# Kernel optimization log

Hardware: AMD Instinct MI355X
Metric: run time of the kernel (lower is better)

The kernel has to match this reference:

```python
import jax, jax.numpy as jnp
import numpy as np

HEADS = 8
SR = 2
EPS_BN = 1e-5
EPS_LN = 1e-5


def _conv(x, w, b, stride=1, pad=0):
    y = jax.lax.conv_general_dilated(x, w, (stride, stride), [(pad, pad), (pad, pad)],
                                     dimension_numbers=('NCHW', 'OIHW', 'NCHW'))
    return y + b[None, :, None, None]


def _bn(x, g, b):
    # eval-mode BatchNorm with running_mean=0, running_var=1
    return x * (g / jnp.sqrt(1.0 + EPS_BN))[None, :, None, None] + b[None, :, None, None]


def _dwt_haar(x):
    # [B,c,H,W] -> [B,4c,H/2,W/2] stacked as LL,HL,LH,HH (Wave-ViT convention)
    x1 = x[:, :, 0::2, 0::2] / 2
    x2 = x[:, :, 1::2, 0::2] / 2
    x3 = x[:, :, 0::2, 1::2] / 2
    x4 = x[:, :, 1::2, 1::2] / 2
    ll = x1 + x2 + x3 + x4
    hl = -x1 - x2 + x3 + x4
    lh = -x1 + x2 - x3 + x4
    hh = x1 - x2 - x3 + x4
    return jnp.concatenate([ll, hl, lh, hh], axis=1)


def _idwt_haar(y):
    # [B,4c,h,w] -> [B,c,2h,2w], exact inverse of _dwt_haar
    c = y.shape[1] // 4
    ll, hl, lh, hh = y[:, :c], y[:, c:2 * c], y[:, 2 * c:3 * c], y[:, 3 * c:]
    p1 = (ll - hl - lh + hh) / 2  # (0::2, 0::2)
    p2 = (ll - hl + lh - hh) / 2  # (1::2, 0::2)
    p3 = (ll + hl - lh - hh) / 2  # (0::2, 1::2)
    p4 = (ll + hl + lh + hh) / 2  # (1::2, 1::2)
    B, _, h2, w2 = ll.shape
    row0 = jnp.stack([p1, p3], axis=-1)  # even rows
    row1 = jnp.stack([p2, p4], axis=-1)  # odd rows
    out = jnp.stack([row0, row1], axis=3)  # [B,c,h2,2,w2,2]
    return out.reshape(B, c, 2 * h2, 2 * w2)


def setup_inputs() -> dict:
    key = jax.random.key(0)
    ks = jax.random.split(key, 12)
    B, H, W, C = 8, 56, 56, 512
    N = H * W
    c4 = C // 4

    def nrm(k, shp, std):
        return jax.random.normal(k, shp, jnp.float32) * std

    return {
        'x': jax.random.normal(ks[0], (B, N, C), jnp.float32),
        'H': H, 'W': W,
        'reduce_w': nrm(ks[1], (c4, C, 1, 1), (2.0 / c4) ** 0.5),
        'reduce_b': jnp.zeros((c4,), jnp.float32),
        'reduce_g': jnp.ones((c4,), jnp.float32),
        'reduce_beta': jnp.zeros((c4,), jnp.float32),
        'filter_w': nrm(ks[2], (C, C, 3, 3), (2.0 / (9 * C)) ** 0.5),
        'filter_b': jnp.zeros((C,), jnp.float32),
        'filter_g': jnp.ones((C,), jnp.float32),
        'filter_beta': jnp.zeros((C,), jnp.float32),
        'q_w': nrm(ks[3], (C, C), 0.02),
        'q_b': jnp.zeros((C,), jnp.float32),
        'ln_g': jnp.ones((C,), jnp.float32),
        'ln_b': jnp.zeros((C,), jnp.float32),
        'kv_w': nrm(ks[4], (2 * C, C), 0.02),
        'kv_b': jnp.zeros((2 * C,), jnp.float32),
        'kve_w': nrm(ks[5], (C, C, SR, SR), (2.0 / (SR * SR * C)) ** 0.5),
        'kve_b': jnp.zeros((C,), jnp.float32),
        'proj_w': nrm(ks[6], (C, C + c4), 0.02),
        'proj_b': jnp.zeros((C,), jnp.float32),
    }


def reference(x, H, W, reduce_w, reduce_b, reduce_g, reduce_beta,
              filter_w, filter_b, filter_g, filter_beta,
              q_w, q_b, ln_g, ln_b, kv_w, kv_b, kve_w, kve_b, proj_w, proj_b):
    B, N, C = x.shape
    hd = C // HEADS
    scale = hd ** -0.5

    q = (x @ q_w.T + q_b).reshape(B, N, HEADS, hd).transpose(0, 2, 1, 3)  # [B,h,N,d]

    xi = x.reshape(B, H, W, C).transpose(0, 3, 1, 2)  # NCHW
    r = jax.nn.relu(_bn(_conv(xi, reduce_w, reduce_b), reduce_g, reduce_beta))  # [B,C/4,H,W]
    r16 = r.astype(jnp.float16)
    x_dwt = _dwt_haar(r16).astype(jnp.float32)  # [B,C,H/2,W/2]
    x_dwt = jax.nn.relu(_bn(_conv(x_dwt, filter_w, filter_b, pad=1), filter_g, filter_beta))
    x_dwt16 = x_dwt.astype(jnp.float16)
    x_idwt = _idwt_haar(x_dwt16)  # [B,C/4,H,W] fp16
    x_idwt = x_idwt.reshape(B, C // 4, H * W).transpose(0, 2, 1)  # [B,N,C/4]

    x_dwt = x_dwt16.astype(jnp.float32)
    kv_in = _conv(x_dwt, kve_w, kve_b, stride=SR).reshape(B, C, -1).transpose(0, 2, 1)  # [B,M,C]
    mu = kv_in.mean(-1, keepdims=True)
    var = ((kv_in - mu) ** 2).mean(-1, keepdims=True)
    kv_n = (kv_in - mu) / jnp.sqrt(var + EPS_LN) * ln_g + ln_b
    kv = (kv_n @ kv_w.T + kv_b).reshape(B, -1, 2, HEADS, hd).transpose(2, 0, 3, 1, 4)
    k, v = kv[0], kv[1]  # [B,h,M,d]

    attn = jax.nn.softmax(jnp.einsum('bhnd,bhmd->bhnm', q, k) * scale, axis=-1)
    o = jnp.einsum('bhnm,bhmd->bhnd', attn, v).transpose(0, 2, 1, 3).reshape(B, N, C)
    o = jnp.concatenate([o, x_idwt.astype(jnp.float32)], axis=-1)  # [B,N,C+C/4]
    return o @ proj_w.T + proj_b
```

## Files before the change

### kernel.cpp

```cpp
#include <hip/hip_runtime.h>
#include <math.h>


typedef _Float16 half8 __attribute__((ext_vector_type(8)));
typedef _Float16 half4v __attribute__((ext_vector_type(4)));
typedef float f32x4 __attribute__((ext_vector_type(4)));

static const size_t OFF_X16  = 0;
static const size_t OFF_Q16  = 12845056;
static const size_t OFF_CAT  = 25690112;
static const size_t OFF_R16  = 41746432;
static const size_t OFF_PAD  = 44957696;
static const size_t OFF_DWTB = 48644096;
static const size_t OFF_QRW  = 51855360;
static const size_t OFF_LN16 = 55066624;
static const size_t OFF_KV16 = 55869440;
static const size_t OFF_WT   = 57475072;
static const size_t OFF_KT   = 59834368;
static const size_t OFF_QW   = 60882944;
static const size_t OFF_KVW  = 61145088;
static const size_t OFF_PW   = 61669376;
static const size_t OFF_RW   = 61997056;
static const size_t OFF_VT   = 62062592;
static const size_t OFF_PART = 62980096;

#define BN_RSQ 0.9999950000374997f
#define SCL2   0.1803368801111204f
#define PART_STRIDE 3211264
#define KVE_STRIDE  802816

__device__ __forceinline__ void async_copy16(const _Float16* g, _Float16* l) {
    __builtin_amdgcn_global_load_lds(
        (const __attribute__((address_space(1))) void*)g,
        (__attribute__((address_space(3))) void*)l, 16, 0, 0);
}

#define WAIT4_BARRIER() asm volatile("s_waitcnt vmcnt(4)\n\ts_barrier" ::: "memory")
#define WAIT0_BARRIER() asm volatile("s_waitcnt vmcnt(0)\n\ts_barrier" ::: "memory")

template <int ALOAD, int EPI>
__global__ __launch_bounds__(256) void gemm16(
    const _Float16* __restrict__ A, const _Float16* __restrict__ W,
    void* __restrict__ outp, int M, int K, int lda, int ldc,
    const float* __restrict__ bias, const float* __restrict__ bng,
    const float* __restrict__ bnb, const float* __restrict__ bias2,
    void* __restrict__ outp2)
{
    __shared__ _Float16 sA[3][128 * 32];
    __shared__ _Float16 sB[3][128 * 32];
    const int t = threadIdx.x;
    const int lane = t & 63, wid = t >> 6;

    int bx = blockIdx.x, by = blockIdx.y;
    {
        int nwg = gridDim.x * gridDim.y;
        if ((nwg & 7) == 0) {
            int orig = by * gridDim.x + bx;
            int cs = nwg >> 3;
            int wg = (orig & 7) * cs + (orig >> 3);
            by = wg % gridDim.y;
            bx = wg / gridDim.y;
        }
    }
    const int m0 = bx * 128, n0 = by * 128;
    const int kbase = blockIdx.z * K;

    const int sr = wid * 16 + (lane >> 2);
    const int sc = (lane & 3) * 8;
    const int stA0 = wid * 512;
    const int stA1 = 2048 + wid * 512;

    const _Float16 *aP0, *aP1;
    if constexpr (ALOAD == 0) {
        int r0 = m0 + sr;      if (r0 > M - 1) r0 = M - 1;
        int r1 = m0 + 64 + sr; if (r1 > M - 1) r1 = M - 1;
        aP0 = A + (size_t)r0 * lda + sc;
        aP1 = A + (size_t)r1 * lda + sc;
    } else {
        int m_ = m0 + sr; if (m_ > M - 1) m_ = M - 1;
        int b_ = m_ / 196, rem = m_ - b_ * 196, i_ = rem / 14, j_ = rem - i_ * 14;
        aP0 = A + ((size_t)(b_ * 784 + 2 * i_ * 28 + 2 * j_)) * 512 + sc;
        m_ = m0 + 64 + sr; if (m_ > M - 1) m_ = M - 1;
        b_ = m_ / 196; rem = m_ - b_ * 196; i_ = rem / 14; j_ = rem - i_ * 14;
        aP1 = A + ((size_t)(b_ * 784 + 2 * i_ * 28 + 2 * j_)) * 512 + sc;
    }
    const int ldw = (ALOAD == 2) ? lda : K;
    const _Float16* bP0 = W + (size_t)(n0 + sr) * ldw + sc;
    const _Float16* bP1 = W + (size_t)(n0 + 64 + sr) * ldw + sc;

    const int mw = wid & 1, nw = wid >> 1;
    const int pAoff = (mw * 64 + (lane & 15)) * 32 + (lane >> 4) * 8;
    const int pBoff = (nw * 64 + (lane & 15)) * 32 + (lane >> 4) * 8;

    f32x4 acc[4][4];
#pragma unroll
    for (int i = 0; i < 4; ++i)
#pragma unroll
        for (int j = 0; j < 4; ++j) acc[i][j] = (f32x4)(0.0f);

    auto aoff_of = [&](int k) -> int {
        if constexpr (ALOAD == 0) {
            return k;
        } else {
            int sub = k >> 9; int ky = sub >> 1, kx = sub & 1;
            return (ky * 28 + kx) * 512 + (k & 511);
        }
    };
    auto stage = [&](int ti, int buf) {
        int k = kbase + ti * 32;
        int aOff = aoff_of(k);
        async_copy16(aP0 + aOff, &sA[buf][stA0]);
        async_copy16(aP1 + aOff, &sA[buf][stA1]);
        async_copy16(bP0 + k, &sB[buf][stA0]);
        async_copy16(bP1 + k, &sB[buf][stA1]);
    };

    const int nt = K >> 5;
    stage(0, 0);
    if (nt > 1) { stage(1, 1); WAIT4_BARRIER(); }
    else        { WAIT0_BARRIER(); }

    int cur = 0;
    for (int i = 0; i < nt; ++i) {
        const _Float16* pA = &sA[cur][0] + pAoff;
        const _Float16* pB = &sB[cur][0] + pBoff;
        half8 aF[4], bF[4];
#pragma unroll
        for (int u = 0; u < 4; ++u) aF[u] = *(const half8*)(pA + u * 512);
#pragma unroll
        for (int u = 0; u < 4; ++u) bF[u] = *(const half8*)(pB + u * 512);

        const bool st = (i + 2 < nt);
        if (st) {
            int nb = cur + 2; if (nb >= 3) nb -= 3;
            stage(i + 2, nb);
        }
#pragma unroll
        for (int u = 0; u < 4; ++u)
#pragma unroll
            for (int j = 0; j < 4; ++j)
                acc[u][j] = __builtin_amdgcn_mfma_f32_16x16x32_f16(
                    aF[u], bF[j], acc[u][j], 0, 0, 0);

        if (i + 1 < nt) {
            if (st) WAIT4_BARRIER();
            else    WAIT0_BARRIER();
        }
        ++cur; if (cur == 3) cur = 0;
    }

    const int orow = m0 + mw * 64 + (lane >> 4) * 4;
    const int ocol = n0 + nw * 64 + (lane & 15);
#pragma unroll
    for (int j = 0; j < 4; ++j) {
        int col = ocol + j * 16;
        float bv = 0.0f, g = 0.0f, b2 = 0.0f;
        if constexpr (EPI == 4) {
            if (n0 >= 512) {
                bv = bias2[col - 512];
                g = bng[col - 512] * BN_RSQ;
                b2 = bnb[col - 512];
            } else {
                bv = bias[col];
            }
        } else if constexpr (EPI != 3) {
            bv = bias[col];
        }
        if constexpr (EPI == 1) { g = bng[col] * BN_RSQ; b2 = bnb[col]; }
#pragma unroll
        for (int i = 0; i < 4; ++i) {
#pragma unroll
            for (int r = 0; r < 4; ++r) {
                int row = orow + i * 16 + r;
                if (row >= M) continue;
                float v = acc[i][j][r] + bv;
                if constexpr (EPI == 1) v = fmaxf(v * g + b2, 0.0f);
                if constexpr (EPI == 0) {
                    __builtin_nontemporal_store(
                        v, (float*)outp + (size_t)row * ldc + col);
                } else if constexpr (EPI == 3) {
                    __builtin_nontemporal_store(
                        v, (float*)outp + (size_t)blockIdx.z * KVE_STRIDE
                           + (size_t)row * ldc + col);
                } else if constexpr (EPI == 4) {
                    if (n0 >= 512) {
                        v = fmaxf(v * g + b2, 0.0f);
                        ((_Float16*)outp2)[(size_t)row * 128 + (col - 512)] =
                            (_Float16)v;
                    } else {
                        ((_Float16*)outp)[(size_t)row * ldc + col] = (_Float16)v;
                    }
                } else {
                    ((_Float16*)outp)[(size_t)row * ldc + col] = (_Float16)v;
                }
            }
        }
    }
}

__global__ __launch_bounds__(256) void conv_splitk(
    const _Float16* __restrict__ A, const _Float16* __restrict__ W,
    float* __restrict__ partA, float* __restrict__ partB)
{
    __shared__ _Float16 sA[3][128 * 32];
    __shared__ _Float16 sB[3][128 * 32];
    const int t = threadIdx.x;
    const int lane = t & 63, wid = t >> 6;

    int orig = blockIdx.x;
    int wg = (orig & 7) * 98 + (orig >> 3);
    int bx = wg % 49;  int c = wg / 49;
    int by = c & 3,    bz = c >> 2;

    const int m0 = bx * 128, n0 = by * 128;
    const int kbase = bz * 1152;

    const int sr = wid * 16 + (lane >> 2);
    const int sc = (lane & 3) * 8;
    const int stA0 = wid * 512;
    const int stA1 = 2048 + wid * 512;

    int m_ = m0 + sr;
    int b_ = m_ / 784, rem = m_ - b_ * 784, y_ = rem / 28, x_ = rem - y_ * 28;
    const _Float16* aP0 = A + ((size_t)(b_ * 900 + (y_ + 1) * 30 + (x_ + 1))) * 512 + sc;
    m_ = m0 + 64 + sr;
    b_ = m_ / 784; rem = m_ - b_ * 784; y_ = rem / 28; x_ = rem - y_ * 28;
    const _Float16* aP1 = A + ((size_t)(b_ * 900 + (y_ + 1) * 30 + (x_ + 1))) * 512 + sc;
    const _Float16* bP0 = W + (size_t)(n0 + sr) * 4608 + sc;
    const _Float16* bP1 = W + (size_t)(n0 + 64 + sr) * 4608 + sc;

    const int mw = wid & 1, nw = wid >> 1;
    const int pAoff = (mw * 64 + (lane & 15)) * 32 + (lane >> 4) * 8;
    const int pBoff = (nw * 64 + (lane & 15)) * 32 + (lane >> 4) * 8;

    f32x4 acc[4][4];
#pragma unroll
    for (int i = 0; i < 4; ++i)
#pragma unroll
        for (int j = 0; j < 4; ++j) acc[i][j] = (f32x4)(0.0f);

    auto aoff_of = [&](int k) -> int {
        int sub = k >> 9; int s3 = sub / 3;
        int dy = s3 - 1, dx = sub - s3 * 3 - 1;
        return (dy * 30 + dx) * 512 + (k & 511);
    };
    auto stage = [&](int ti, int buf) {
        int k = kbase + ti * 32;
        int aOff = aoff_of(k);
        async_copy16(aP0 + aOff, &sA[buf][stA0]);
        async_copy16(aP1 + aOff, &sA[buf][stA1]);
        async_copy16(bP0 + k, &sB[buf][stA0]);
        async_copy16(bP1 + k, &sB[buf][stA1]);
    };

    const int nt = 36;
    stage(0, 0);
    stage(1, 1);
    WAIT4_BARRIER();

    int cur = 0;
    for (int i = 0; i < nt; ++i) {
        const _Float16* pA = &sA[cur][0] + pAoff;
        const _Float16* pB = &sB[cur][0] + pBoff;
        half8 aF[4], bF[4];
#pragma unroll
        for (int u = 0; u < 4; ++u) aF[u] = *(const half8*)(pA + u * 512);
#pragma unroll
        for (int u = 0; u < 4; ++u) bF[u] = *(const half8*)(pB + u * 512);

        const bool st = (i + 2 < nt);
        if (st) {
            int nb = cur + 2; if (nb >= 3) nb -= 3;
            stage(i + 2, nb);
        }
#pragma unroll
        for (int u = 0; u < 4; ++u)
#pragma unroll
            for (int j = 0; j < 4; ++j)
                acc[u][j] = __builtin_amdgcn_mfma_f32_16x16x32_f16(
                    aF[u], bF[j], acc[u][j], 0, 0, 0);

        if (i + 1 < nt) {
            if (st) WAIT4_BARRIER();
            else    WAIT0_BARRIER();
        }
        ++cur; if (cur == 3) cur = 0;
    }

    float* dst = (bz < 2) ? (partA + (size_t)bz * PART_STRIDE)
                          : (partB + (size_t)(bz - 2) * PART_STRIDE);
    const int orow = m0 + mw * 64 + (lane >> 4) * 4;
    const int ocol = n0 + nw * 64 + (lane & 15);
#pragma unroll
    for (int j = 0; j < 4; ++j) {
#pragma unroll
        for (int i = 0; i < 4; ++i)
#pragma unroll
            for (int r = 0; r < 4; ++r)
                __builtin_nontemporal_store(
                    acc[i][j][r],
                    &dst[(size_t)(orow + i * 16 + r) * 512 + ocol + j * 16]);
    }
}

__global__ __launch_bounds__(256) void conv_epi(
    const float* __restrict__ pA, const float* __restrict__ pB,
    _Float16* __restrict__ o, const float* __restrict__ bias,
    const float* __restrict__ bng, const float* __restrict__ bnb)
{
    int i = blockIdx.x * 256 + threadIdx.x;
    size_t base = (size_t)i * 8;
    int c = (int)(base & 511);
    half8 hv;
#pragma unroll
    for (int u = 0; u < 8; u += 4) {
        f32x4 a0 = __builtin_nontemporal_load((const f32x4*)(pA + base + u));
        f32x4 a1 = __builtin_nontemporal_load((const f32x4*)(pA + PART_STRIDE + base + u));
        f32x4 a2 = __builtin_nontemporal_load((const f32x4*)(pB + base + u));
        f32x4 a3 = __builtin_nontemporal_load((const f32x4*)(pB + PART_STRIDE + base + u));
#pragma unroll
        for (int v = 0; v < 4; ++v) {
            int cc = c + u + v;
            float s = (a0[v] + a1[v]) + (a2[v] + a3[v]);
            float val = (s + bias[cc]) * (bng[cc] * BN_RSQ) + bnb[cc];
            hv[u + v] = (_Float16)fmaxf(val, 0.0f);
        }
    }
    *(half8*)(o + base) = hv;
}

__global__ __launch_bounds__(256) void cvt_f32_f16(
    const float* __restrict__ s, _Float16* __restrict__ d, int n8)
{
    int i = blockIdx.x * 256 + threadIdx.x;
    if (i >= n8) return;
    const float4* sp = (const float4*)(s + (size_t)i * 8);
    float4 a = sp[0], b = sp[1];
    half8 h;
    h[0] = (_Float16)a.x; h[1] = (_Float16)a.y; h[2] = (_Float16)a.z; h[3] = (_Float16)a.w;
    h[4] = (_Float16)b.x; h[5] = (_Float16)b.y; h[6] = (_Float16)b.z; h[7] = (_Float16)b.w;
    *(half8*)(d + (size_t)i * 8) = h;
}

__global__ __launch_bounds__(256) void zero_half(_Float16* __restrict__ p, int n8)
{
    int i = blockIdx.x * 256 + threadIdx.x;
    if (i < n8) *(float4*)(p + (size_t)i * 8) = make_float4(0.f, 0.f, 0.f, 0.f);
}

__global__ __launch_bounds__(256) void transpose_filter16(
    const float* __restrict__ fw, _Float16* __restrict__ wT)
{
    int idx = blockIdx.x * 256 + threadIdx.x;
    int n = idx / 4608; int r = idx - n * 4608;
    int sub = r >> 9; int ci = r & 511;
    wT[idx] = (_Float16)fw[(size_t)n * 4608 + ci * 9 + sub];
}

__global__ __launch_bounds__(256) void transpose_kve16(
    const float* __restrict__ kw, _Float16* __restrict__ kT)
{
    int idx = blockIdx.x * 256 + threadIdx.x;
    int n = idx >> 11; int r = idx & 2047;
    int sub = r >> 9; int ci = r & 511;
    kT[idx] = (_Float16)kw[((size_t)n << 11) + (ci << 2) + sub];
}

__global__ __launch_bounds__(256) void vt_prep(
    const _Float16* __restrict__ kv, _Float16* __restrict__ vt)
{
    int idx = blockIdx.x * 256 + threadIdx.x;
    int m = idx % 224;
    int rest = idx / 224;
    int d = rest & 63;
    int bh = rest >> 6;
    int b = bh >> 3, h = bh & 7;
    _Float16 v = (_Float16)0.0f;
    if (m < 196)
        v = kv[((size_t)(b * 196 + m)) * 1024 + 512 + h * 64 + d];
    vt[idx] = v;
}

__global__ __launch_bounds__(128) void dwt_kernel(
    const _Float16* __restrict__ r, _Float16* __restrict__ pad)
{
    int bid = blockIdx.x;
    int b = bid / 784; int rem = bid - b * 784;
    int i = rem / 28;  int j = rem - i * 28;
    int c = threadIdx.x;
    int y = 2 * i, x = 2 * j;
    size_t base = (size_t)b * 3136;
    _Float16 f1 = r[(base + (size_t)y * 56 + x) * 128 + c];
    _Float16 f2 = r[(base + (size_t)(y + 1) * 56 + x) * 128 + c];
    _Float16 f3 = r[(base + (size_t)y * 56 + (x + 1)) * 128 + c];
    _Float16 f4 = r[(base + (size_t)(y + 1) * 56 + (x + 1)) * 128 + c];
    _Float16 h = (_Float16)0.5f;
    _Float16 x1 = f1 * h, x2 = f2 * h, x3 = f3 * h, x4 = f4 * h;
    _Float16 ll = ((x1 + x2) + x3) + x4;
    _Float16 hl = (((-x1) - x2) + x3) + x4;
    _Float16 lh = (((-x1) + x2) - x3) + x4;
    _Float16 hh = ((x1 - x2) - x3) + x4;
    size_t ob = ((size_t)b * 900 + (size_t)(i + 1) * 30 + (j + 1)) * 512;
    pad[ob + c]       = ll;
    pad[ob + 128 + c] = hl;
    pad[ob + 256 + c] = lh;
    pad[ob + 384 + c] = hh;
}

__global__ __launch_bounds__(128) void idwt_kernel(
    const _Float16* __restrict__ d, _Float16* __restrict__ cat)
{
    int bid = blockIdx.x;
    int b = bid / 784; int rem = bid - b * 784;
    int i = rem / 28;  int j = rem - i * 28;
    int c = threadIdx.x;
    size_t ib = ((size_t)b * 784 + (size_t)i * 28 + j) * 512;
    _Float16 ll = d[ib + c];
    _Float16 hl = d[ib + 128 + c];
    _Float16 lh = d[ib + 256 + c];
    _Float16 hh = d[ib + 384 + c];
    _Float16 h = (_Float16)0.5f;
    _Float16 p1 = (((ll - hl) - lh) + hh) * h;
    _Float16 p2 = (((ll - hl) + lh) - hh) * h;
    _Float16 p3 = (((ll + hl) - lh) - hh) * h;
    _Float16 p4 = (((ll + hl) + lh) + hh) * h;
    int y = 2 * i, x = 2 * j;
    size_t rb = (size_t)b * 3136;
    __builtin_nontemporal_store(p1, &cat[(rb + (size_t)y * 56 + x) * 640 + 512 + c]);
    __builtin_nontemporal_store(p3, &cat[(rb + (size_t)y * 56 + x + 1) * 640 + 512 + c]);
    __builtin_nontemporal_store(p2, &cat[(rb + (size_t)(y + 1) * 56 + x) * 640 + 512 + c]);
    __builtin_nontemporal_store(p4, &cat[(rb + (size_t)(y + 1) * 56 + x + 1) * 640 + 512 + c]);
}

__global__ __launch_bounds__(256) void ln_kernel(
    const float* __restrict__ part, _Float16* __restrict__ o,
    const float* __restrict__ g, const float* __restrict__ bta,
    const float* __restrict__ kvb)
{
    int wave = threadIdx.x >> 6;
    int lane = threadIdx.x & 63;
    int row = blockIdx.x * 4 + wave;
    int c = lane * 8;
    const float* rp = part + (size_t)row * 512 + c;
    float v[8];
#pragma unroll
    for (int i = 0; i < 8; i += 4) {
        float4 a0 = *(const float4*)(rp + i);
        float4 a1 = *(const float4*)(rp + KVE_STRIDE + i);
        float4 a2 = *(const float4*)(rp + 2 * KVE_STRIDE + i);
        float4 a3 = *(const float4*)(rp + 3 * KVE_STRIDE + i);
        v[i + 0] = (a0.x + a1.x) + (a2.x + a3.x) + kvb[c + i + 0];
        v[i + 1] = (a0.y + a1.y) + (a2.y + a3.y) + kvb[c + i + 1];
        v[i + 2] = (a0.z + a1.z) + (a2.z + a3.z) + kvb[c + i + 2];
        v[i + 3] = (a0.w + a1.w) + (a2.w + a3.w) + kvb[c + i + 3];
    }
    float s = ((v[0] + v[1]) + (v[2] + v[3])) + ((v[4] + v[5]) + (v[6] + v[7]));
#pragma unroll
    for (int off = 32; off; off >>= 1) s += __shfl_xor(s, off);
    float mu = s * (1.0f / 512.0f);
    float sq = 0.0f;
#pragma unroll
    for (int i = 0; i < 8; ++i) { v[i] -= mu; sq += v[i] * v[i]; }
#pragma unroll
    for (int off = 32; off; off >>= 1) sq += __shfl_xor(sq, off);
    float inv = 1.0f / sqrtf(sq * (1.0f / 512.0f) + 1e-5f);
    half8 hv;
#pragma unroll
    for (int i = 0; i < 8; ++i) hv[i] = (_Float16)(v[i] * inv * g[c + i] + bta[c + i]);
    *(half8*)(o + (size_t)row * 512 + c) = hv;
}

__global__ __launch_bounds__(256) void attn_mfma(
    const _Float16* __restrict__ q, const _Float16* __restrict__ kv,
    const _Float16* __restrict__ vt, _Float16* __restrict__ cat)
{
    __shared__ _Float16 sK[64][72];
    __shared__ _Float16 sVT[64][72];
    __shared__ _Float16 sP[4][16][40];
    int bid = blockIdx.x;
    int qt = bid % 49;
    int h  = (bid / 49) & 7;
    int b  = bid / 392;
    int n0 = qt * 64;
    int t = threadIdx.x, lane = t & 63, wid = t >> 6;
    int quad = lane >> 4, l16 = lane & 15;

    const _Float16* qp = q + ((size_t)(b * 3136 + n0 + wid * 16 + l16)) * 512
                           + h * 64 + quad * 8;
    half8 aQ0 = *(const half8*)qp;
    half8 aQ1 = *(const half8*)(qp + 32);

    f32x4 oacc[4];
#pragma unroll
    for (int i = 0; i < 4; ++i) oacc[i] = (f32x4)(0.0f);
    float lsum[4] = {0.f, 0.f, 0.f, 0.f};

    const _Float16* vtb = vt + ((size_t)((b * 8 + h) * 64)) * 224;

    for (int c0 = 0; c0 < 224; c0 += 64) {
        __syncthreads();
#pragma unroll
        for (int it = 0; it < 2; ++it) {
            int slot = t + 256 * it;
            int row = slot >> 3, c8 = (slot & 7) * 8;
            int m = c0 + row; if (m > 195) m = 195;
            *(half8*)&sK[row][c8] =
                *(const half8*)(kv + ((size_t)(b * 196 + m)) * 1024 + h * 64 + c8);
        }
#pragma unroll
        for (int it = 0; it < 2; ++it) {
            int slot = t + 256 * it;
            int row = slot >> 3, c8 = (slot & 7) * 8;
            *(half8*)&sVT[row][c8] =
                *(const half8*)(vtb + (size_t)row * 224 + c0 + c8);
        }
        __syncthreads();

#pragma unroll
        for (int sc = 0; sc < 64; sc += 32) {
            half8 bk00 = *(const half8*)&sK[sc + l16][quad * 8];
            half8 bk01 = *(const half8*)&sK[sc + l16][32 + quad * 8];
            half8 bk10 = *(const half8*)&sK[sc + 16 + l16][quad * 8];
            half8 bk11 = *(const half8*)&sK[sc + 16 + l16][32 + quad * 8];
            f32x4 s0 = (f32x4)(0.0f), s1 = (f32x4)(0.0f);
            s0 = __builtin_amdgcn_mfma_f32_16x16x32_f16(aQ0, bk00, s0, 0, 0, 0);
            s0 = __builtin_amdgcn_mfma_f32_16x16x32_f16(aQ1, bk01, s0, 0, 0, 0);
            s1 = __builtin_amdgcn_mfma_f32_16x16x32_f16(aQ0, bk10, s1, 0, 0, 0);
            s1 = __builtin_amdgcn_mfma_f32_16x16x32_f16(aQ1, bk11, s1, 0, 0, 0);

            int col0 = c0 + sc + l16;
            float msk0 = (col0 < 196) ? 0.0f : -INFINITY;
            float msk1 = (col0 + 16 < 196) ? 0.0f : -INFINITY;
            float p0[4], p1[4];
#pragma unroll
            for (int r = 0; r < 4; ++r) {
                p0[r] = exp2f(s0[r] * SCL2 + msk0);
                p1[r] = exp2f(s1[r] * SCL2 + msk1);
                lsum[r] += p0[r] + p1[r];
            }
#pragma unroll
            for (int r = 0; r < 4; ++r) {
                sP[wid][quad * 4 + r][l16]      = (_Float16)p0[r];
                sP[wid][quad * 4 + r][16 + l16] = (_Float16)p1[r];
            }
            half8 aP = *(const half8*)&sP[wid][l16][quad * 8];
            half8 bv0 = *(const half8*)&sVT[l16][sc + quad * 8];
            half8 bv1 = *(const half8*)&sVT[16 + l16][sc + quad * 8];
            half8 bv2 = *(const half8*)&sVT[32 + l16][sc + quad * 8];
            half8 bv3 = *(const half8*)&sVT[48 + l16][sc + quad * 8];
            oacc[0] = __builtin_amdgcn_mfma_f32_16x16x32_f16(aP, bv0, oacc[0], 0, 0, 0);
            oacc[1] = __builtin_amdgcn_mfma_f32_16x16x32_f16(aP, bv1, oacc[1], 0, 0, 0);
            oacc[2] = __builtin_amdgcn_mfma_f32_16x16x32_f16(aP, bv2, oacc[2], 0, 0, 0);
            oacc[3] = __builtin_amdgcn_mfma_f32_16x16x32_f16(aP, bv3, oacc[3], 0, 0, 0);
        }
    }

    float inv[4];
#pragma unroll
    for (int r = 0; r < 4; ++r) {
        float s = lsum[r];
        s += __shfl_xor(s, 1);
        s += __shfl_xor(s, 2);
        s += __shfl_xor(s, 4);
        s += __shfl_xor(s, 8);
        inv[r] = 1.0f / s;
    }
#pragma unroll
    for (int r = 0; r < 4; ++r) {
        size_t rowoff = ((size_t)(b * 3136 + n0 + wid * 16 + quad * 4 + r)) * 640
                        + h * 64 + l16;
#pragma unroll
        for (int tv = 0; tv < 4; ++tv)
            __builtin_nontemporal_store(
                (_Float16)(oacc[tv][r] * inv[r]), &cat[rowoff + tv * 16]);
    }
}

extern "C" void kernel_launch(void* const* d_in, const int* in_sizes, int n_in,
                              void* d_out, int out_size, void* d_ws, size_t ws_size,
                              hipStream_t stream)
{
    const float* x           = (const float*)d_in[0];
    const float* reduce_w    = (const float*)d_in[3];
    const float* reduce_b    = (const float*)d_in[4];
    const float* reduce_g    = (const float*)d_in[5];
    const float* reduce_beta = (const float*)d_in[6];
    const float* filter_w    = (const float*)d_in[7];
    const float* filter_b    = (const float*)d_in[8];
    const float* filter_g    = (const float*)d_in[9];
    const float* filter_beta = (const float*)d_in[10];
    const float* q_w         = (const float*)d_in[11];
    const float* q_b         = (const float*)d_in[12];
    const float* ln_g        = (const float*)d_in[13];
    const float* ln_b        = (const float*)d_in[14];
    const float* kv_w        = (const float*)d_in[15];
    const float* kv_b        = (const float*)d_in[16];
    const float* kve_w       = (const float*)d_in[17];
    const float* kve_b       = (const float*)d_in[18];
    const float* proj_w      = (const float*)d_in[19];
    const float* proj_b      = (const float*)d_in[20];
    float* out = (float*)d_out;
    _Float16* hws = (_Float16*)d_ws;

    _Float16* x16    = hws + OFF_X16;
    _Float16* q16    = hws + OFF_Q16;
    _Float16* cat16  = hws + OFF_CAT;
    _Float16* r16    = hws + OFF_R16;
    _Float16* pad16  = hws + OFF_PAD;
    _Float16* dwtb16 = hws + OFF_DWTB;
    _Float16* qrw16  = hws + OFF_QRW;
    _Float16* ln16   = hws + OFF_LN16;
    _Float16* kv16   = hws + OFF_KV16;
    _Float16* wT16   = hws + OFF_WT;
    _Float16* kT16   = hws + OFF_KT;
    _Float16* kvw16  = hws + OFF_KVW;
    _Float16* pw16   = hws + OFF_PW;
    _Float16* vt16   = hws + OFF_VT;
    float*    partA  = (float*)(hws + OFF_X16);
    float*    partB  = (float*)(hws + OFF_PART);
    float*    kvepart = (float*)(hws + OFF_X16);

    cvt_f32_f16<<<dim3(6272), dim3(256), 0, stream>>>(x, x16, 1605632);
    cvt_f32_f16<<<dim3(128),  dim3(256), 0, stream>>>(q_w, qrw16, 32768);
    cvt_f32_f16<<<dim3(32),   dim3(256), 0, stream>>>(reduce_w, qrw16 + 262144, 8192);
    cvt_f32_f16<<<dim3(256),  dim3(256), 0, stream>>>(kv_w, kvw16, 65536);
    cvt_f32_f16<<<dim3(160),  dim3(256), 0, stream>>>(proj_w, pw16, 40960);
    transpose_filter16<<<dim3(9216), dim3(256), 0, stream>>>(filter_w, wT16);
    transpose_kve16<<<dim3(4096), dim3(256), 0, stream>>>(kve_w, kT16);
    zero_half<<<dim3(1800), dim3(256), 0, stream>>>(pad16, 460800);

    gemm16<0, 4><<<dim3(196, 5), dim3(256), 0, stream>>>(
        x16, qrw16, q16, 25088, 512, 512, 512, q_b, reduce_g, reduce_beta,
        reduce_b, r16);

    dwt_kernel<<<dim3(6272), dim3(128), 0, stream>>>(r16, pad16);

    conv_splitk<<<dim3(784), dim3(256), 0, stream>>>(pad16, wT16, partA, partB);
    conv_epi<<<dim3(1568), dim3(256), 0, stream>>>(
        partA, partB, dwtb16, filter_b, filter_g, filter_beta);

    idwt_kernel<<<dim3(6272), dim3(128), 0, stream>>>(dwtb16, cat16);

    gemm16<2, 3><<<dim3(13, 4, 4), dim3(256), 0, stream>>>(
        dwtb16, kT16, kvepart, 1568, 512, 2048, 512, nullptr, nullptr, nullptr,
        nullptr, nullptr);

    ln_kernel<<<dim3(392), dim3(256), 0, stream>>>(kvepart, ln16, ln_g, ln_b, kve_b);

    gemm16<0, 2><<<dim3(13, 8), dim3(256), 0, stream>>>(
        ln16, kvw16, kv16, 1568, 512, 512, 1024, kv_b, nullptr, nullptr,
        nullptr, nullptr);

    vt_prep<<<dim3(3584), dim3(256), 0, stream>>>(kv16, vt16);

    attn_mfma<<<dim3(3136), dim3(256), 0, stream>>>(q16, kv16, vt16, cat16);

    gemm16<0, 0><<<dim3(196, 4), dim3(256), 0, stream>>>(
        cat16, pw16, out, 25088, 640, 640, 512, proj_b, nullptr, nullptr,
        nullptr, nullptr);
}
```

Measured before the change: 411.2 us.

## Fuse weight prep kernels, conv epilogue with IDWT, and V-transpose into KV GEMM

Merges the weight conversion, transposition and zero-fill launches into a single prep kernel. Fuses the split-K conv reduction and BN/ReLU epilogue with the inverse Haar transform, so the filtered tensor is not re-read. Adds a GEMM epilogue that writes V directly in transposed layout, which removes the vt_prep kernel; vt is zero-filled up front so the padded columns stay zero. Several nontemporal stores are also turned into ordinary stores. Together these cut launch count and intermediate traffic, at the risk of scattered 2-byte stores in the V-transpose epilogue.

```diff
diff --git a/kernel.cpp b/kernel.cpp
--- a/kernel.cpp
+++ b/kernel.cpp
@@ -3,7 +3,6 @@
 
 
 typedef _Float16 half8 __attribute__((ext_vector_type(8)));
-typedef _Float16 half4v __attribute__((ext_vector_type(4)));
 typedef float f32x4 __attribute__((ext_vector_type(4)));
 
 static const size_t OFF_X16  = 0;
@@ -17,10 +16,8 @@
 static const size_t OFF_KV16 = 55869440;
 static const size_t OFF_WT   = 57475072;
 static const size_t OFF_KT   = 59834368;
-static const size_t OFF_QW   = 60882944;
 static const size_t OFF_KVW  = 61145088;
 static const size_t OFF_PW   = 61669376;
-static const size_t OFF_RW   = 61997056;
 static const size_t OFF_VT   = 62062592;
 static const size_t OFF_PART = 62980096;
 
@@ -166,7 +163,6 @@
         } else if constexpr (EPI != 3) {
             bv = bias[col];
         }
-        if constexpr (EPI == 1) { g = bng[col] * BN_RSQ; b2 = bnb[col]; }
 #pragma unroll
         for (int i = 0; i < 4; ++i) {
 #pragma unroll
@@ -174,19 +170,27 @@
                 int row = orow + i * 16 + r;
                 if (row >= M) continue;
                 float v = acc[i][j][r] + bv;
-                if constexpr (EPI == 1) v = fmaxf(v * g + b2, 0.0f);
                 if constexpr (EPI == 0) {
                     __builtin_nontemporal_store(
                         v, (float*)outp + (size_t)row * ldc + col);
                 } else if constexpr (EPI == 3) {
-                    __builtin_nontemporal_store(
-                        v, (float*)outp + (size_t)blockIdx.z * KVE_STRIDE
-                           + (size_t)row * ldc + col);
+                    ((float*)outp)[(size_t)blockIdx.z * KVE_STRIDE
+                                   + (size_t)row * ldc + col] = v;
                 } else if constexpr (EPI == 4) {
                     if (n0 >= 512) {
                         v = fmaxf(v * g + b2, 0.0f);
                         ((_Float16*)outp2)[(size_t)row * 128 + (col - 512)] =
                             (_Float16)v;
+                    } else {
+                        ((_Float16*)outp)[(size_t)row * ldc + col] = (_Float16)v;
+                    }
+                } else if constexpr (EPI == 5) {
+                    if (n0 >= 512) {
+                        int hd_ = col - 512;
+                        int h_ = hd_ >> 6, d_ = hd_ & 63;
+                        int b_ = row / 196, m_ = row - b_ * 196;
+                        ((_Float16*)outp2)[((size_t)((b_ * 8 + h_) * 64 + d_)) * 224
+                                           + m_] = (_Float16)v;
                     } else {
                         ((_Float16*)outp)[(size_t)row * ldc + col] = (_Float16)v;
                     }
@@ -297,43 +301,48 @@
         for (int i = 0; i < 4; ++i)
 #pragma unroll
             for (int r = 0; r < 4; ++r)
-                __builtin_nontemporal_store(
-                    acc[i][j][r],
-                    &dst[(size_t)(orow + i * 16 + r) * 512 + ocol + j * 16]);
-    }
-}
-
-__global__ __launch_bounds__(256) void conv_epi(
+                dst[(size_t)(orow + i * 16 + r) * 512 + ocol + j * 16] = acc[i][j][r];
+    }
+}
+
+__global__ __launch_bounds__(128) void conv_epi_idwt(
     const float* __restrict__ pA, const float* __restrict__ pB,
-    _Float16* __restrict__ o, const float* __restrict__ bias,
-    const float* __restrict__ bng, const float* __restrict__ bnb)
-{
-    int i = blockIdx.x * 256 + threadIdx.x;
-    size_t base = (size_t)i * 8;
-    int c = (int)(base & 511);
-    half8 hv;
-#pragma unroll
-    for (int u = 0; u < 8; u += 4) {
-        f32x4 a0 = __builtin_nontemporal_load((const f32x4*)(pA + base + u));
-        f32x4 a1 = __builtin_nontemporal_load((const f32x4*)(pA + PART_STRIDE + base + u));
-        f32x4 a2 = __builtin_nontemporal_load((const f32x4*)(pB + base + u));
-        f32x4 a3 = __builtin_nontemporal_load((const f32x4*)(pB + PART_STRIDE + base + u));
-#pragma unroll
-        for (int v = 0; v < 4; ++v) {
-            int cc = c + u + v;
-            float s = (a0[v] + a1[v]) + (a2[v] + a3[v]);
-            float val = (s + bias[cc]) * (bng[cc] * BN_RSQ) + bnb[cc];
-            hv[u + v] = (_Float16)fmaxf(val, 0.0f);
-        }
-    }
-    *(half8*)(o + base) = hv;
-}
-
-__global__ __launch_bounds__(256) void cvt_f32_f16(
-    const float* __restrict__ s, _Float16* __restrict__ d, int n8)
-{
-    int i = blockIdx.x * 256 + threadIdx.x;
-    if (i >= n8) return;
+    _Float16* __restrict__ dwtb, _Float16* __restrict__ cat,
+    const float* __restrict__ bias, const float* __restrict__ bng,
+    const float* __restrict__ bnb)
+{
+    int p = blockIdx.x;
+    int b = p / 784; int rem = p - b * 784;
+    int i = rem / 28;  int j = rem - i * 28;
+    int c = threadIdx.x;
+    size_t base = (size_t)p * 512;
+    _Float16 g16[4];
+#pragma unroll
+    for (int g = 0; g < 4; ++g) {
+        int ch = g * 128 + c;
+        float s = (pA[base + ch] + pA[PART_STRIDE + base + ch])
+                + (pB[base + ch] + pB[PART_STRIDE + base + ch]);
+        float v = (s + bias[ch]) * (bng[ch] * BN_RSQ) + bnb[ch];
+        g16[g] = (_Float16)fmaxf(v, 0.0f);
+        dwtb[base + ch] = g16[g];
+    }
+    _Float16 ll = g16[0], hl = g16[1], lh = g16[2], hh = g16[3];
+    _Float16 h = (_Float16)0.5f;
+    _Float16 p1 = (((ll - hl) - lh) + hh) * h;
+    _Float16 p2 = (((ll - hl) + lh) - hh) * h;
+    _Float16 p3 = (((ll + hl) - lh) - hh) * h;
+    _Float16 p4 = (((ll + hl) + lh) + hh) * h;
+    int y = 2 * i, x = 2 * j;
+    size_t rb = (size_t)b * 3136;
+    __builtin_nontemporal_store(p1, &cat[(rb + (size_t)y * 56 + x) * 640 + 512 + c]);
+    __builtin_nontemporal_store(p3, &cat[(rb + (size_t)y * 56 + x + 1) * 640 + 512 + c]);
+    __builtin_nontemporal_store(p2, &cat[(rb + (size_t)(y + 1) * 56 + x) * 640 + 512 + c]);
+    __builtin_nontemporal_store(p4, &cat[(rb + (size_t)(y + 1) * 56 + x + 1) * 640 + 512 + c]);
+}
+
+__device__ __forceinline__ void cvt8_at(
+    const float* __restrict__ s, _Float16* __restrict__ d, int i)
+{
     const float4* sp = (const float4*)(s + (size_t)i * 8);
     float4 a = sp[0], b = sp[1];
     half8 h;
@@ -342,43 +351,49 @@
     *(half8*)(d + (size_t)i * 8) = h;
 }
 
-__global__ __launch_bounds__(256) void zero_half(_Float16* __restrict__ p, int n8)
+__global__ __launch_bounds__(256) void prep_kernel(
+    const float* __restrict__ qw, const float* __restrict__ rw,
+    const float* __restrict__ kvw, const float* __restrict__ pw,
+    const float* __restrict__ fw, const float* __restrict__ kw,
+    _Float16* __restrict__ qrw16, _Float16* __restrict__ kvw16,
+    _Float16* __restrict__ pw16, _Float16* __restrict__ wT,
+    _Float16* __restrict__ kT, _Float16* __restrict__ pad,
+    _Float16* __restrict__ vt)
+{
+    int bid = blockIdx.x, tid = threadIdx.x;
+    if (bid < 128) {
+        cvt8_at(qw, qrw16, bid * 256 + tid);
+    } else if (bid < 160) {
+        cvt8_at(rw, qrw16 + 262144, (bid - 128) * 256 + tid);
+    } else if (bid < 416) {
+        cvt8_at(kvw, kvw16, (bid - 160) * 256 + tid);
+    } else if (bid < 576) {
+        cvt8_at(pw, pw16, (bid - 416) * 256 + tid);
+    } else if (bid < 9792) {
+        int idx = (bid - 576) * 256 + tid;
+        int n = idx / 4608; int r = idx - n * 4608;
+        int sub = r >> 9; int ci = r & 511;
+        wT[idx] = (_Float16)fw[(size_t)n * 4608 + ci * 9 + sub];
+    } else if (bid < 13888) {
+        int idx = (bid - 9792) * 256 + tid;
+        int n = idx >> 11; int r = idx & 2047;
+        int sub = r >> 9; int ci = r & 511;
+        kT[idx] = (_Float16)kw[((size_t)n << 11) + (ci << 2) + sub];
+    } else if (bid < 15688) {
+        int i = (bid - 13888) * 256 + tid;
+        *(float4*)(pad + (size_t)i * 8) = make_float4(0.f, 0.f, 0.f, 0.f);
+    } else {
+        int i = (bid - 15688) * 256 + tid;
+        *(float4*)(vt + (size_t)i * 8) = make_float4(0.f, 0.f, 0.f, 0.f);
+    }
+}
+
+__global__ __launch_bounds__(256) void cvt_f32_f16(
+    const float* __restrict__ s, _Float16* __restrict__ d, int n8)
 {
     int i = blockIdx.x * 256 + threadIdx.x;
-    if (i < n8) *(float4*)(p + (size_t)i * 8) = make_float4(0.f, 0.f, 0.f, 0.f);
-}
-
-__global__ __launch_bounds__(256) void transpose_filter16(
-    const float* __restrict__ fw, _Float16* __restrict__ wT)
-{
-    int idx = blockIdx.x * 256 + threadIdx.x;
-    int n = idx / 4608; int r = idx - n * 4608;
-    int sub = r >> 9; int ci = r & 511;
-    wT[idx] = (_Float16)fw[(size_t)n * 4608 + ci * 9 + sub];
-}
-
-__global__ __launch_bounds__(256) void transpose_kve16(
-    const float* __restrict__ kw, _Float16* __restrict__ kT)
-{
-    int idx = blockIdx.x * 256 + threadIdx.x;
-    int n = idx >> 11; int r = idx & 2047;
-    int sub = r >> 9; int ci = r & 511;
-    kT[idx] = (_Float16)kw[((size_t)n << 11) + (ci << 2) + sub];
-}
-
-__global__ __launch_bounds__(256) void vt_prep(
-    const _Float16* __restrict__ kv, _Float16* __restrict__ vt)
-{
-    int idx = blockIdx.x * 256 + threadIdx.x;
-    int m = idx % 224;
-    int rest = idx / 224;
-    int d = rest & 63;
-    int bh = rest >> 6;
-    int b = bh >> 3, h = bh & 7;
-    _Float16 v = (_Float16)0.0f;
-    if (m < 196)
-        v = kv[((size_t)(b * 196 + m)) * 1024 + 512 + h * 64 + d];
-    vt[idx] = v;
+    if (i >= n8) return;
+    cvt8_at(s, d, i);
 }
 
 __global__ __launch_bounds__(128) void dwt_kernel(
@@ -407,31 +422,6 @@
     pad[ob + 384 + c] = hh;
 }
 
-__global__ __launch_bounds__(128) void idwt_kernel(
-    const _Float16* __restrict__ d, _Float16* __restrict__ cat)
-{
-    int bid = blockIdx.x;
-    int b = bid / 784; int rem = bid - b * 784;
-    int i = rem / 28;  int j = rem - i * 28;
-    int c = threadIdx.x;
-    size_t ib = ((size_t)b * 784 + (size_t)i * 28 + j) * 512;
-    _Float16 ll = d[ib + c];
-    _Float16 hl = d[ib + 128 + c];
-    _Float16 lh = d[ib + 256 + c];
-    _Float16 hh = d[ib + 384 + c];
-    _Float16 h = (_Float16)0.5f;
-    _Float16 p1 = (((ll - hl) - lh) + hh) * h;
-    _Float16 p2 = (((ll - hl) + lh) - hh) * h;
-    _Float16 p3 = (((ll + hl) - lh) - hh) * h;
-    _Float16 p4 = (((ll + hl) + lh) + hh) * h;
-    int y = 2 * i, x = 2 * j;
-    size_t rb = (size_t)b * 3136;
-    __builtin_nontemporal_store(p1, &cat[(rb + (size_t)y * 56 + x) * 640 + 512 + c]);
-    __builtin_nontemporal_store(p3, &cat[(rb + (size_t)y * 56 + x + 1) * 640 + 512 + c]);
-    __builtin_nontemporal_store(p2, &cat[(rb + (size_t)(y + 1) * 56 + x) * 640 + 512 + c]);
-    __builtin_nontemporal_store(p4, &cat[(rb + (size_t)(y + 1) * 56 + x + 1) * 640 + 512 + c]);
-}
-
 __global__ __launch_bounds__(256) void ln_kernel(
     const float* __restrict__ part, _Float16* __restrict__ o,
     const float* __restrict__ g, const float* __restrict__ bta,
@@ -571,8 +561,7 @@
                         + h * 64 + l16;
 #pragma unroll
         for (int tv = 0; tv < 4; ++tv)
-            __builtin_nontemporal_store(
-                (_Float16)(oacc[tv][r] * inv[r]), &cat[rowoff + tv * 16]);
+            cat[rowoff + tv * 16] = (_Float16)(oacc[tv][r] * inv[r]);
     }
 }
 
@@ -620,14 +609,11 @@
     float*    partB  = (float*)(hws + OFF_PART);
     float*    kvepart = (float*)(hws + OFF_X16);
 
+    prep_kernel<<<dim3(16136), dim3(256), 0, stream>>>(
+        q_w, reduce_w, kv_w, proj_w, filter_w, kve_w,
+        qrw16, kvw16, pw16, wT16, kT16, pad16, vt16);
+
     cvt_f32_f16<<<dim3(6272), dim3(256), 0, stream>>>(x, x16, 1605632);
-    cvt_f32_f16<<<dim3(128),  dim3(256), 0, stream>>>(q_w, qrw16, 32768);
-    cvt_f32_f16<<<dim3(32),   dim3(256), 0, stream>>>(reduce_w, qrw16 + 262144, 8192);
-    cvt_f32_f16<<<dim3(256),  dim3(256), 0, stream>>>(kv_w, kvw16, 65536);
-    cvt_f32_f16<<<dim3(160),  dim3(256), 0, stream>>>(proj_w, pw16, 40960);
-    transpose_filter16<<<dim3(9216), dim3(256), 0, stream>>>(filter_w, wT16);
-    transpose_kve16<<<dim3(4096), dim3(256), 0, stream>>>(kve_w, kT16);
-    zero_half<<<dim3(1800), dim3(256), 0, stream>>>(pad16, 460800);
 
     gemm16<0, 4><<<dim3(196, 5), dim3(256), 0, stream>>>(
         x16, qrw16, q16, 25088, 512, 512, 512, q_b, reduce_g, reduce_beta,
@@ -636,10 +622,9 @@
     dwt_kernel<<<dim3(6272), dim3(128), 0, stream>>>(r16, pad16);
 
     conv_splitk<<<dim3(784), dim3(256), 0, stream>>>(pad16, wT16, partA, partB);
-    conv_epi<<<dim3(1568), dim3(256), 0, stream>>>(
-        partA, partB, dwtb16, filter_b, filter_g, filter_beta);
-
-    idwt_kernel<<<dim3(6272), dim3(128), 0, stream>>>(dwtb16, cat16);
+
+    conv_epi_idwt<<<dim3(6272), dim3(128), 0, stream>>>(
+        partA, partB, dwtb16, cat16, filter_b, filter_g, filter_beta);
 
     gemm16<2, 3><<<dim3(13, 4, 4), dim3(256), 0, stream>>>(
         dwtb16, kT16, kvepart, 1568, 512, 2048, 512, nullptr, nullptr, nullptr,
@@ -647,11 +632,9 @@
 
     ln_kernel<<<dim3(392), dim3(256), 0, stream>>>(kvepart, ln16, ln_g, ln_b, kve_b);
 
-    gemm16<0, 2><<<dim3(13, 8), dim3(256), 0, stream>>>(
+    gemm16<0, 5><<<dim3(13, 8), dim3(256), 0, stream>>>(
         ln16, kvw16, kv16, 1568, 512, 512, 1024, kv_b, nullptr, nullptr,
-        nullptr, nullptr);
-
-    vt_prep<<<dim3(3584), dim3(256), 0, stream>>>(kv16, vt16);
+        nullptr, vt16);
 
     attn_mfma<<<dim3(3136), dim3(256), 0, stream>>>(q16, kv16, vt16, cat16);
 
```

Measured after the change: 399.0 us. -3.0%, faster.
